# Kernel optimization log

Hardware: AMD Instinct MI355X
Metric: run time of the kernel (lower is better)

Reference implementation:

```python
import jax, jax.numpy as jnp
import numpy as np

C, PH, PW, H, W = 10, 7, 7, 34, 34
STRIDE = 8.0
S = 4  # sample_per_part


def setup_inputs() -> dict:
    key = jax.random.key(0)
    k1, k2, k3, k4, k5 = jax.random.split(key, 5)
    N = 30000
    ft = jax.random.normal(k1, (1, C * PH * PW, H, W), dtype=jnp.float32)
    x1 = jax.random.uniform(k2, (N,), dtype=jnp.float32) * 200.0
    y1 = jax.random.uniform(k3, (N,), dtype=jnp.float32) * 200.0
    bw = jax.random.uniform(k4, (N,), dtype=jnp.float32) * 70.0 + 2.0
    bh = jax.random.uniform(k5, (N,), dtype=jnp.float32) * 70.0 + 2.0
    rois = jnp.stack([jnp.zeros((N,), jnp.float32), x1, y1, x1 + bw, y1 + bh], axis=1)
    return {"ft_add_left_right": ft, "rois": rois}


def reference(ft_add_left_right, rois):
    ft = ft_add_left_right[0].reshape(C, PH, PW, H, W)
    roi_start_w = rois[:, 1] / STRIDE
    roi_start_h = rois[:, 2] / STRIDE
    roi_end_w = rois[:, 3] / STRIDE
    roi_end_h = rois[:, 4] / STRIDE
    # torch.threshold(x, 0.1, 0.1): x if x > 0.1 else 0.1
    roi_height = jnp.where(roi_end_h - roi_start_h > 0.1, roi_end_h - roi_start_h, 0.1)
    roi_width = jnp.where(roi_end_w - roi_start_w > 0.1, roi_end_w - roi_start_w, 0.1)
    bin_size_h = roi_height / PH
    bin_size_w = roi_width / PW
    sub_h = bin_size_h / S
    sub_w = bin_size_w / S

    gh, gw = jnp.meshgrid(jnp.arange(PH), jnp.arange(PW), indexing='ij')
    phs = gh.reshape(-1, 1)  # [49,1]
    pws = gw.reshape(-1, 1)  # [49,1]
    hstart = jnp.floor(roi_start_h + phs * bin_size_h)  # [49,N]
    wstart = jnp.floor(roi_start_w + pws * bin_size_w)  # [49,N]

    N = rois.shape[0]
    sum_ = jnp.zeros((C, PH * PW, N), jnp.float32)
    count = jnp.zeros((PH * PW, N), jnp.float32)

    for ih in range(S):
        for iw in range(S):
            w = wstart + (iw + 0.5) * sub_w  # [49,N]
            h = hstart + (ih + 0.5) * sub_h
            keep = (w > -1) & (w < W) & (h > -1) & (h < H)
            x1 = jnp.floor(w).astype(jnp.int32)
            x2 = jnp.ceil(w).astype(jnp.int32)
            y1 = jnp.floor(h).astype(jnp.int32)
            y2 = jnp.ceil(h).astype(jnp.int32)
            x1v = (x1 >= 0) & (x1 < W)
            x2v = (x2 >= 0) & (x2 < W)
            y1v = (y1 >= 0) & (y1 < H)
            y2v = (y2 >= 0) & (y2 < H)
            x1 = jnp.clip(x1, 0, W - 1)
            x2 = jnp.clip(x2, 0, W - 1)
            y1 = jnp.clip(y1, 0, H - 1)
            y2 = jnp.clip(y2, 0, H - 1)
            dist_x = w - x1
            dist_y = h - y1
            # gathers: result [C,49,N]
            v11 = ft[:, phs, pws, y1, x1]
            v12 = ft[:, phs, pws, y2, x1]
            v21 = ft[:, phs, pws, y1, x2]
            v22 = ft[:, phs, pws, y2, x2]
            # faithful to source: ALL four masks zero value11 only (source bug)
            bad11 = (~x1v & y1v) | (~x1v & y2v) | (~x2v & y1v) | (~x2v & y2v)
            v11 = jnp.where(bad11, 0.0, v11)
            value = ((1 - dist_x) * (1 - dist_y) * v11
                     + (1 - dist_x) * dist_y * v12
                     + dist_x * (1 - dist_y) * v21
                     + dist_x * dist_y * v22)
            sum_ = sum_ + jnp.where(keep, value, 0.0)
            count = count + keep.astype(jnp.float32)

    out = jnp.where(count > 0, sum_ / jnp.maximum(count, 1.0), sum_)
    return jnp.transpose(out, (2, 0, 1))  # [N, C, 49]
```

## Files before the change

### kernel.cpp

```cpp
#include <hip/hip_runtime.h>
#include <hip/hip_fp16.h>


#define NC 10
#define NBIN 49
#define FH 34
#define FW 34
#define PLANE (FH * FW)
#define NPIX (NBIN * PLANE)
#define GPC 18882
#define RPB 16
#define TSTRIDE 491
#define NSIDE 14

__global__ __launch_bounds__(256) void prep_kernel(
    const float* __restrict__ ft, unsigned int* __restrict__ ftR)
{
    const int p = blockIdx.x * 256 + threadIdx.x;
    if (p >= NPIX + 2) return;
    unsigned int h2[5];
    if (p < NPIX) {
#pragma unroll
        for (int c = 0; c < 5; ++c) {
            const __half lo = __float2half_rn(ft[(2 * c)     * NPIX + p]);
            const __half hi = __float2half_rn(ft[(2 * c + 1) * NPIX + p]);
            const __half2 hh = __halves2half2(lo, hi);
            h2[c] = *(const unsigned int*)&hh;
        }
    } else {
#pragma unroll
        for (int c = 0; c < 5; ++c) h2[c] = 0u;
    }
#pragma unroll
    for (int m = 0; m < 3; ++m) {
        if (p >= m) {
            const int t = p - m;
            const int g = t / 3;
            const int j = t - 3 * g;
            if (g < GPC) {
                unsigned int* d = ftR + ((size_t)m * GPC + g) * 16 + j * 5;
#pragma unroll
                for (int c = 0; c < 5; ++c) d[c] = h2[c];
            }
        }
    }
}

__device__ __forceinline__ void fma2(float w, unsigned int u, float& s0, float& s1)
{
    const __half2 h = *(const __half2*)&u;
    s0 = fmaf(w, __half2float(__low2half(h)),  s0);
    s1 = fmaf(w, __half2float(__high2half(h)), s1);
}

__global__ __launch_bounds__(256, 4) void main_kernel(
    const float* __restrict__ rois, const unsigned int* __restrict__ ftR,
    const float* __restrict__ ft, float* __restrict__ out, int N, int use_t)
{
    __shared__ float sides[NSIDE][RPB][8];
    __shared__ float tile[RPB][TSTRIDE];

    const int r = threadIdx.x & (RPB - 1);
    const int s = threadIdx.x >> 4;
    const int n = blockIdx.x * RPB + r;
    const bool valid = (n < N);

    float rsw = 0.f, rsh = 0.f, rew = 0.f, reh = 0.f;
    if (valid) {
        rsw = rois[n * 5 + 1] * 0.125f;
        rsh = rois[n * 5 + 2] * 0.125f;
        rew = rois[n * 5 + 3] * 0.125f;
        reh = rois[n * 5 + 4] * 0.125f;
    }
    float rheight = __fsub_rn(reh, rsh);
    if (!(rheight > 0.1f)) rheight = 0.1f;
    float rwidth = __fsub_rn(rew, rsw);
    if (!(rwidth > 0.1f)) rwidth = 0.1f;
    const float bsh   = __fdiv_rn(rheight, 7.0f);
    const float bsw   = __fdiv_rn(rwidth, 7.0f);
    const float sub_h = __fdiv_rn(bsh, 4.0f);
    const float sub_w = __fdiv_rn(bsw, 4.0f);

    if (s < NSIDE) {
        const bool isY = (s < 7);
        const int  k   = isY ? s : s - 7;
        const float st = isY ? rsh : rsw;
        const float bs = isY ? bsh : bsw;
        const float sb = isY ? sub_h : sub_w;
        const float start = floorf(__fadd_rn(st, __fmul_rn((float)k, bs)));

        float A[3] = {0.f, 0.f, 0.f}, B[3] = {0.f, 0.f, 0.f};
        float cnt = 0.f;
        int P0 = 0;
#pragma unroll
        for (int i = 0; i < 4; ++i) {
            const float h = __fadd_rn(start, __fmul_rn((float)i + 0.5f, sb));
            const bool ok = (h > -1.0f) && (h < 34.0f);
            const int p1 = (int)floorf(h);
            const int p2 = (int)ceilf(h);
            const bool v1 = (p1 >= 0) && (p1 < 34);
            const bool v2 = (p2 >= 0) && (p2 < 34);
            const int p1c = min(max(p1, 0), 33);
            const int p2c = min(max(p2, 0), 33);
            const float d = __fsub_rn(h, (float)p1c);
            if (i == 0) P0 = p1c;
            const int i1 = p1c - P0, i2 = p2c - P0;
            const float t1 = ok ? (1.0f - d) : 0.0f;
            const float t2 = ok ? d : 0.0f;
            const bool bsel = isY ? (v1 || v2) : ((!v1) || (!v2));
            const float tb = (ok && bsel) ? (1.0f - d) : 0.0f;
            cnt += ok ? 1.0f : 0.0f;
#pragma unroll
            for (int p = 0; p < 3; ++p) {
                A[p] += (i1 == p) ? t1 : 0.0f;
                A[p] += (i2 == p) ? t2 : 0.0f;
                B[p] += (i1 == p) ? tb : 0.0f;
            }
        }
        float* sp = &sides[s][r][0];
        sp[0] = A[0]; sp[1] = A[1]; sp[2] = A[2];
        sp[3] = B[0]; sp[4] = B[1]; sp[5] = B[2];
        sp[6] = cnt;  sp[7] = (float)P0;
    }
    __syncthreads();

#pragma unroll
    for (int j = 0; j < 4; ++j) {
        const int bin = j * RPB + s;
        if (valid && bin < NBIN) {
            const int ph = bin / 7;
            const int pw = bin - ph * 7;

            const float4 ya = *(const float4*)&sides[ph][r][0];
            const float4 yb = *(const float4*)&sides[ph][r][4];
            const float4 xa = *(const float4*)&sides[7 + pw][r][0];
            const float4 xb = *(const float4*)&sides[7 + pw][r][4];
            const float AY[3] = {ya.x, ya.y, ya.z};
            const float BY[3] = {ya.w, yb.x, yb.y};
            const float cntY  = yb.z;
            const int   Y0    = (int)yb.w;
            const float AX[3] = {xa.x, xa.y, xa.z};
            const float BX[3] = {xa.w, xb.x, xb.y};
            const float cntX  = xb.z;
            const int   X0    = (int)xb.w;

            const int binbase = bin * PLANE;
            const int rowo[3] = {binbase + Y0 * FW,
                                 binbase + min(Y0 + 1, FH - 1) * FW,
                                 binbase + min(Y0 + 2, FH - 1) * FW};

            float wgt[9];
#pragma unroll
            for (int p = 0; p < 3; ++p)
#pragma unroll
                for (int q = 0; q < 3; ++q)
                    wgt[3 * p + q] = AY[p] * AX[q] - BY[p] * BX[q];

            float sum[NC];
#pragma unroll
            for (int c = 0; c < NC; ++c) sum[c] = 0.f;

            if (use_t) {
                const int e = (FW - 1) - X0;
                unsigned int rv[3][15];
                float ew[3][3];
#pragma unroll
                for (int p = 0; p < 3; ++p) {
                    const float w0 = wgt[3 * p], w1 = wgt[3 * p + 1], w2 = wgt[3 * p + 2];
                    const float s12 = w1 + w2;
                    ew[p][0] = (e < 1) ? (w0 + s12) : w0;
                    ew[p][1] = (e < 1) ? 0.f : ((e < 2) ? s12 : w1);
                    ew[p][2] = (e < 2) ? 0.f : w2;
                    const bool rnz = (w0 != 0.0f) || (w1 != 0.0f) || (w2 != 0.0f);
                    const int fp = rnz ? (rowo[p] + X0) : binbase;
                    const int g = fp / 3;
                    const int m = fp - 3 * g;
                    const unsigned int* lp = ftR + ((size_t)m * GPC + g) * 16;
                    const uint4 a = *(const uint4*)lp;
                    const uint4 b = *(const uint4*)(lp + 4);
                    const uint4 c4 = *(const uint4*)(lp + 8);
                    const uint4 d4 = *(const uint4*)(lp + 12);
                    rv[p][0]  = a.x;  rv[p][1]  = a.y;  rv[p][2]  = a.z;  rv[p][3]  = a.w;
                    rv[p][4]  = b.x;  rv[p][5]  = b.y;  rv[p][6]  = b.z;  rv[p][7]  = b.w;
                    rv[p][8]  = c4.x; rv[p][9]  = c4.y; rv[p][10] = c4.z; rv[p][11] = c4.w;
                    rv[p][12] = d4.x; rv[p][13] = d4.y; rv[p][14] = d4.z;
                }
#pragma unroll
                for (int p = 0; p < 3; ++p)
#pragma unroll
                    for (int c = 0; c < 5; ++c) {
                        fma2(ew[p][0], rv[p][c],      sum[2 * c], sum[2 * c + 1]);
                        fma2(ew[p][1], rv[p][5 + c],  sum[2 * c], sum[2 * c + 1]);
                        fma2(ew[p][2], rv[p][10 + c], sum[2 * c], sum[2 * c + 1]);
                    }
            } else {
                const int colo[3] = {X0, min(X0 + 1, FW - 1), min(X0 + 2, FW - 1)};
                int off[9];
#pragma unroll
                for (int p = 0; p < 3; ++p)
#pragma unroll
                    for (int q = 0; q < 3; ++q)
                        off[3 * p + q] = (wgt[3 * p + q] != 0.0f) ? (rowo[p] + colo[q])
                                                                  : binbase;
#pragma unroll
                for (int k = 0; k < 9; ++k) {
                    const float w = wgt[k];
#pragma unroll
                    for (int c = 0; c < NC; ++c)
                        sum[c] = fmaf(w, ft[c * NPIX + off[k]], sum[c]);
                }
            }

            const float cnt = cntY * cntX;
            const float inv = (cnt > 0.0f) ? __fdiv_rn(1.0f, cnt) : 1.0f;
            float* tp = &tile[r][0];
#pragma unroll
            for (int c = 0; c < NC; ++c) tp[c * NBIN + bin] = sum[c] * inv;
        }
    }

    __syncthreads();

    const int n0 = blockIdx.x * RPB;
    for (int i = threadIdx.x; i < RPB * (NC * NBIN); i += 256) {
        const int row = i / (NC * NBIN);
        const int col = i - row * (NC * NBIN);
        const int n2 = n0 + row;
        if (n2 < N) out[(size_t)n2 * (NC * NBIN) + col] = tile[row][col];
    }
}

extern "C" void kernel_launch(void* const* d_in, const int* in_sizes, int n_in,
                              void* d_out, int out_size, void* d_ws, size_t ws_size,
                              hipStream_t stream) {
    const float* ft   = (const float*)d_in[0];
    const float* rois = (const float*)d_in[1];
    float* out        = (float*)d_out;
    const int N = in_sizes[1] / 5;

    const size_t need = (size_t)3 * GPC * 64;
    const int use_t = (ws_size >= need) ? 1 : 0;
    unsigned int* ftR = (unsigned int*)d_ws;

    if (use_t) {
        prep_kernel<<<(NPIX + 2 + 255) / 256, 256, 0, stream>>>(ft, ftR);
    }
    main_kernel<<<(N + RPB - 1) / RPB, 256, 0, stream>>>(rois, ftR, ft, out, N, use_t);
}
```

Measured before the change: 114.8 us.

## Sort ROIs by spatial key and remap blocks per XCD for cache locality

Adds a counting sort of ROIs keyed on start cell, half-cell parity and size class (histogram, scan, scatter kernels), so each block processes spatially similar ROIs. Block indices are also remapped so that consecutive sorted ranges land on the same XCD, which is meant to improve L2 reuse of the gathered feature data. The cost is four extra small kernel launches, a single-block serial scan, and output rows now written scattered through the permutation instead of contiguously.

```diff
diff --git a/kernel.cpp b/kernel.cpp
--- a/kernel.cpp
+++ b/kernel.cpp
@@ -12,6 +12,8 @@
 #define RPB 16
 #define TSTRIDE 491
 #define NSIDE 14
+#define NBUCKET 65536
+#define NXCD 8
 
 __global__ __launch_bounds__(256) void prep_kernel(
     const float* __restrict__ ft, unsigned int* __restrict__ ftR)
@@ -46,6 +48,71 @@
     }
 }
 
+__device__ __forceinline__ unsigned int roi_key(const float* __restrict__ rois, int n)
+{
+    const float rsw = rois[n * 5 + 1] * 0.125f;
+    const float rsh = rois[n * 5 + 2] * 0.125f;
+    const float rew = rois[n * 5 + 3] * 0.125f;
+    const float reh = rois[n * 5 + 4] * 0.125f;
+    float rh = reh - rsh; if (!(rh > 0.1f)) rh = 0.1f;
+    float rw = rew - rsw; if (!(rw > 0.1f)) rw = 0.1f;
+    const int y0 = min(31, max(0, (int)floorf(rsh)));
+    const int x0 = min(31, max(0, (int)floorf(rsw)));
+    const int yf = ((int)floorf(rsh * 2.0f)) & 1;
+    const int xf = ((int)floorf(rsw * 2.0f)) & 1;
+    const int bh = min(3, (int)(rh * (2.0f / 7.0f)));
+    const int bw = min(3, (int)(rw * (2.0f / 7.0f)));
+    return (unsigned int)((((((((y0 << 5) | x0) << 1) | yf) << 1) | xf) << 2 | bh) << 2 | bw);
+}
+
+__global__ __launch_bounds__(256) void zero_kernel(unsigned int* __restrict__ cursor)
+{
+    cursor[blockIdx.x * 256 + threadIdx.x] = 0u;
+}
+
+__global__ __launch_bounds__(256) void hist_kernel(
+    const float* __restrict__ rois, unsigned int* __restrict__ keys,
+    unsigned int* __restrict__ cursor, int N)
+{
+    const int n = blockIdx.x * 256 + threadIdx.x;
+    if (n >= N) return;
+    const unsigned int k = roi_key(rois, n);
+    keys[n] = k;
+    atomicAdd(&cursor[k], 1u);
+}
+
+__global__ __launch_bounds__(1024) void scan_kernel(unsigned int* __restrict__ cursor)
+{
+    __shared__ unsigned int part[1024];
+    const int t = threadIdx.x;
+    unsigned int s = 0;
+    for (int i = 0; i < 64; ++i) s += cursor[t * 64 + i];
+    part[t] = s;
+    __syncthreads();
+    for (int off = 1; off < 1024; off <<= 1) {
+        const unsigned int v = (t >= off) ? part[t - off] : 0u;
+        __syncthreads();
+        part[t] += v;
+        __syncthreads();
+    }
+    unsigned int ex = (t == 0) ? 0u : part[t - 1];
+    for (int i = 0; i < 64; ++i) {
+        const unsigned int c = cursor[t * 64 + i];
+        cursor[t * 64 + i] = ex;
+        ex += c;
+    }
+}
+
+__global__ __launch_bounds__(256) void scatter_kernel(
+    const unsigned int* __restrict__ keys, unsigned int* __restrict__ cursor,
+    int* __restrict__ perm, int N)
+{
+    const int n = blockIdx.x * 256 + threadIdx.x;
+    if (n >= N) return;
+    const unsigned int pos = atomicAdd(&cursor[keys[n]], 1u);
+    perm[pos] = n;
+}
+
 __device__ __forceinline__ void fma2(float w, unsigned int u, float& s0, float& s1)
 {
     const __half2 h = *(const __half2*)&u;
@@ -55,22 +122,29 @@
 
 __global__ __launch_bounds__(256, 4) void main_kernel(
     const float* __restrict__ rois, const unsigned int* __restrict__ ftR,
-    const float* __restrict__ ft, float* __restrict__ out, int N, int use_t)
+    const int* __restrict__ perm, const float* __restrict__ ft,
+    float* __restrict__ out, int N, int use_t)
 {
     __shared__ float sides[NSIDE][RPB][8];
     __shared__ float tile[RPB][TSTRIDE];
 
+    const int nwg = gridDim.x;
+    const int q = nwg / NXCD, rr = nwg % NXCD;
+    const int xcd = blockIdx.x % NXCD, idx = blockIdx.x / NXCD;
+    const int bid = (xcd < rr ? xcd * (q + 1) : rr * (q + 1) + (xcd - rr) * q) + idx;
+
     const int r = threadIdx.x & (RPB - 1);
     const int s = threadIdx.x >> 4;
-    const int n = blockIdx.x * RPB + r;
+    const int n = bid * RPB + r;
     const bool valid = (n < N);
+    const int nn = (use_t && valid) ? perm[n] : n;
 
     float rsw = 0.f, rsh = 0.f, rew = 0.f, reh = 0.f;
     if (valid) {
-        rsw = rois[n * 5 + 1] * 0.125f;
-        rsh = rois[n * 5 + 2] * 0.125f;
-        rew = rois[n * 5 + 3] * 0.125f;
-        reh = rois[n * 5 + 4] * 0.125f;
+        rsw = rois[nn * 5 + 1] * 0.125f;
+        rsh = rois[nn * 5 + 2] * 0.125f;
+        rew = rois[nn * 5 + 3] * 0.125f;
+        reh = rois[nn * 5 + 4] * 0.125f;
     }
     float rheight = __fsub_rn(reh, rsh);
     if (!(rheight > 0.1f)) rheight = 0.1f;
@@ -153,8 +227,8 @@
 #pragma unroll
             for (int p = 0; p < 3; ++p)
 #pragma unroll
-                for (int q = 0; q < 3; ++q)
-                    wgt[3 * p + q] = AY[p] * AX[q] - BY[p] * BX[q];
+                for (int q2 = 0; q2 < 3; ++q2)
+                    wgt[3 * p + q2] = AY[p] * AX[q2] - BY[p] * BX[q2];
 
             float sum[NC];
 #pragma unroll
@@ -199,9 +273,9 @@
 #pragma unroll
                 for (int p = 0; p < 3; ++p)
 #pragma unroll
-                    for (int q = 0; q < 3; ++q)
-                        off[3 * p + q] = (wgt[3 * p + q] != 0.0f) ? (rowo[p] + colo[q])
-                                                                  : binbase;
+                    for (int q2 = 0; q2 < 3; ++q2)
+                        off[3 * p + q2] = (wgt[3 * p + q2] != 0.0f) ? (rowo[p] + colo[q2])
+                                                                    : binbase;
 #pragma unroll
                 for (int k = 0; k < 9; ++k) {
                     const float w = wgt[k];
@@ -221,12 +295,15 @@
 
     __syncthreads();
 
-    const int n0 = blockIdx.x * RPB;
+    const int n0 = bid * RPB;
     for (int i = threadIdx.x; i < RPB * (NC * NBIN); i += 256) {
         const int row = i / (NC * NBIN);
         const int col = i - row * (NC * NBIN);
         const int n2 = n0 + row;
-        if (n2 < N) out[(size_t)n2 * (NC * NBIN) + col] = tile[row][col];
+        if (n2 < N) {
+            const int nd = use_t ? perm[n2] : n2;
+            out[(size_t)nd * (NC * NBIN) + col] = tile[row][col];
+        }
     }
 }
 
@@ -238,12 +315,20 @@
     float* out        = (float*)d_out;
     const int N = in_sizes[1] / 5;
 
-    const size_t need = (size_t)3 * GPC * 64;
+    const size_t ftr_bytes = (size_t)3 * GPC * 64;
+    const size_t need = ftr_bytes + (size_t)NBUCKET * 4 + (size_t)8 * N;
     const int use_t = (ws_size >= need) ? 1 : 0;
-    unsigned int* ftR = (unsigned int*)d_ws;
+    unsigned int* ftR    = (unsigned int*)d_ws;
+    unsigned int* cursor = (unsigned int*)((char*)d_ws + ftr_bytes);
+    unsigned int* keys   = cursor + NBUCKET;
+    int*          perm   = (int*)(keys + N);
 
     if (use_t) {
         prep_kernel<<<(NPIX + 2 + 255) / 256, 256, 0, stream>>>(ft, ftR);
-    }
-    main_kernel<<<(N + RPB - 1) / RPB, 256, 0, stream>>>(rois, ftR, ft, out, N, use_t);
-}
+        zero_kernel<<<NBUCKET / 256, 256, 0, stream>>>(cursor);
+        hist_kernel<<<(N + 255) / 256, 256, 0, stream>>>(rois, keys, cursor, N);
+        scan_kernel<<<1, 1024, 0, stream>>>(cursor);
+        scatter_kernel<<<(N + 255) / 256, 256, 0, stream>>>(keys, cursor, perm, N);
+    }
+    main_kernel<<<(N + RPB - 1) / RPB, 256, 0, stream>>>(rois, ftR, perm, ft, out, N, use_t);
+}
```

Result: slower. 144.9 us (+26.2%).

## Software-pipeline bin gathers with double-buffered registers and reduce occupancy hint

Applied to the files above, without the earlier changes.

Restructures the per-thread bin loop into a two-stage software pipeline. The gather loads for the next bin are issued before the FMAs of the current bin, using A/B register buffers, so global-memory latency overlaps with arithmetic. Invalid bins are handled by masking the weights and pointing at offset zero, which removes divergent branches around the loads. In exchange, register pressure goes up, so the launch-bounds minimum blocks per SM drops from 4 to 3. The prep kernel also moves to 1024-thread blocks.

```diff
diff --git a/kernel.cpp b/kernel.cpp
--- a/kernel.cpp
+++ b/kernel.cpp
@@ -13,11 +13,9 @@
 #define TSTRIDE 491
 #define NSIDE 14
 
-__global__ __launch_bounds__(256) void prep_kernel(
-    const float* __restrict__ ft, unsigned int* __restrict__ ftR)
-{
-    const int p = blockIdx.x * 256 + threadIdx.x;
-    if (p >= NPIX + 2) return;
+__device__ __forceinline__ void pack_pixel(
+    const float* __restrict__ ft, unsigned int* __restrict__ ftR, int p)
+{
     unsigned int h2[5];
     if (p < NPIX) {
 #pragma unroll
@@ -46,6 +44,13 @@
     }
 }
 
+__global__ __launch_bounds__(1024) void prep_kernel(
+    const float* __restrict__ ft, unsigned int* __restrict__ ftR)
+{
+    const int p = blockIdx.x * 1024 + threadIdx.x;
+    if (p < NPIX + 2) pack_pixel(ft, ftR, p);
+}
+
 __device__ __forceinline__ void fma2(float w, unsigned int u, float& s0, float& s1)
 {
     const __half2 h = *(const __half2*)&u;
@@ -53,7 +58,77 @@
     s1 = fmaf(w, __half2float(__high2half(h)), s1);
 }
 
-__global__ __launch_bounds__(256, 4) void main_kernel(
+
+#define BIN_META(J, EW, FP, INV, BINV, BVV)                                    \
+    {                                                                          \
+        BINV = (J) * RPB + s;                                                  \
+        BVV = valid && (BINV < NBIN);                                          \
+        const float msk = BVV ? 1.0f : 0.0f;                                   \
+        const int ph = BINV / 7;                                               \
+        const int pw = BINV - ph * 7;                                          \
+        const float4 ya = *(const float4*)&sides[ph][r][0];                    \
+        const float4 yb = *(const float4*)&sides[ph][r][4];                    \
+        const float4 xa = *(const float4*)&sides[7 + pw][r][0];                \
+        const float4 xb = *(const float4*)&sides[7 + pw][r][4];                \
+        const float AY[3] = {ya.x, ya.y, ya.z};                                \
+        const float BY[3] = {ya.w, yb.x, yb.y};                                \
+        const float AX[3] = {xa.x, xa.y, xa.z};                                \
+        const float BX[3] = {xa.w, xb.x, xb.y};                                \
+        const int Y0 = (int)yb.w;                                              \
+        const int X0 = (int)xb.w;                                              \
+        const float cnt = yb.z * xb.z;                                         \
+        INV = (cnt > 0.0f) ? __fdiv_rn(1.0f, cnt) : 1.0f;                      \
+        const int binbase = BINV * PLANE;                                      \
+        const int rowo[3] = {binbase + Y0 * FW,                                \
+                             binbase + min(Y0 + 1, FH - 1) * FW,               \
+                             binbase + min(Y0 + 2, FH - 1) * FW};              \
+        const int e = (FW - 1) - X0;                                           \
+        _Pragma("unroll") for (int p = 0; p < 3; ++p) {                        \
+            const float w0 = (AY[p] * AX[0] - BY[p] * BX[0]) * msk;            \
+            const float w1 = (AY[p] * AX[1] - BY[p] * BX[1]) * msk;            \
+            const float w2 = (AY[p] * AX[2] - BY[p] * BX[2]) * msk;            \
+            const float s12 = w1 + w2;                                         \
+            EW[p][0] = (e < 1) ? (w0 + s12) : w0;                              \
+            EW[p][1] = (e < 1) ? 0.f : ((e < 2) ? s12 : w1);                   \
+            EW[p][2] = (e < 2) ? 0.f : w2;                                     \
+            const bool rnz = (w0 != 0.0f) || (w1 != 0.0f) || (w2 != 0.0f);     \
+            FP[p] = BVV ? (rnz ? (rowo[p] + X0) : binbase) : 0;                \
+        }                                                                      \
+    }
+
+#define LOAD3(FP, RV)                                                          \
+    _Pragma("unroll") for (int p = 0; p < 3; ++p) {                            \
+        const int g = FP[p] / 3;                                               \
+        const int m = FP[p] - 3 * g;                                           \
+        const unsigned int* lp = ftR + ((size_t)m * GPC + g) * 16;             \
+        const uint4 a = *(const uint4*)lp;                                     \
+        const uint4 b4 = *(const uint4*)(lp + 4);                              \
+        const uint4 c4 = *(const uint4*)(lp + 8);                              \
+        const uint4 d4 = *(const uint4*)(lp + 12);                             \
+        RV[p][0] = a.x;  RV[p][1] = a.y;  RV[p][2] = a.z;  RV[p][3] = a.w;     \
+        RV[p][4] = b4.x; RV[p][5] = b4.y; RV[p][6] = b4.z; RV[p][7] = b4.w;    \
+        RV[p][8] = c4.x; RV[p][9] = c4.y; RV[p][10] = c4.z; RV[p][11] = c4.w;  \
+        RV[p][12] = d4.x; RV[p][13] = d4.y; RV[p][14] = d4.z;    \
+    }
+
+#define FMA_STORE(EW, RV, INV, BINV, BVV)                                      \
+    {                                                                          \
+        float sum[NC];                                                         \
+        _Pragma("unroll") for (int c = 0; c < NC; ++c) sum[c] = 0.f;           \
+        _Pragma("unroll") for (int p = 0; p < 3; ++p)                          \
+            _Pragma("unroll") for (int c = 0; c < 5; ++c) {                    \
+                fma2(EW[p][0], RV[p][c],      sum[2 * c], sum[2 * c + 1]);     \
+                fma2(EW[p][1], RV[p][5 + c],  sum[2 * c], sum[2 * c + 1]);     \
+                fma2(EW[p][2], RV[p][10 + c], sum[2 * c], sum[2 * c + 1]);     \
+            }                                                                  \
+        if (BVV) {                                                             \
+            float* tp = &tile[r][0];                                           \
+            _Pragma("unroll") for (int c = 0; c < NC; ++c)                     \
+                tp[c * NBIN + BINV] = sum[c] * INV;                            \
+        }                                                                      \
+    }
+
+__global__ __launch_bounds__(256, 3) void main_kernel(
     const float* __restrict__ rois, const unsigned int* __restrict__ ftR,
     const float* __restrict__ ft, float* __restrict__ out, int N, int use_t)
 {
@@ -124,84 +199,61 @@
     }
     __syncthreads();
 
-#pragma unroll
-    for (int j = 0; j < 4; ++j) {
-        const int bin = j * RPB + s;
-        if (valid && bin < NBIN) {
-            const int ph = bin / 7;
-            const int pw = bin - ph * 7;
-
-            const float4 ya = *(const float4*)&sides[ph][r][0];
-            const float4 yb = *(const float4*)&sides[ph][r][4];
-            const float4 xa = *(const float4*)&sides[7 + pw][r][0];
-            const float4 xb = *(const float4*)&sides[7 + pw][r][4];
-            const float AY[3] = {ya.x, ya.y, ya.z};
-            const float BY[3] = {ya.w, yb.x, yb.y};
-            const float cntY  = yb.z;
-            const int   Y0    = (int)yb.w;
-            const float AX[3] = {xa.x, xa.y, xa.z};
-            const float BX[3] = {xa.w, xb.x, xb.y};
-            const float cntX  = xb.z;
-            const int   X0    = (int)xb.w;
-
-            const int binbase = bin * PLANE;
-            const int rowo[3] = {binbase + Y0 * FW,
-                                 binbase + min(Y0 + 1, FH - 1) * FW,
-                                 binbase + min(Y0 + 2, FH - 1) * FW};
-
-            float wgt[9];
-#pragma unroll
-            for (int p = 0; p < 3; ++p)
-#pragma unroll
-                for (int q = 0; q < 3; ++q)
-                    wgt[3 * p + q] = AY[p] * AX[q] - BY[p] * BX[q];
-
-            float sum[NC];
-#pragma unroll
-            for (int c = 0; c < NC; ++c) sum[c] = 0.f;
-
-            if (use_t) {
-                const int e = (FW - 1) - X0;
-                unsigned int rv[3][15];
-                float ew[3][3];
-#pragma unroll
-                for (int p = 0; p < 3; ++p) {
-                    const float w0 = wgt[3 * p], w1 = wgt[3 * p + 1], w2 = wgt[3 * p + 2];
-                    const float s12 = w1 + w2;
-                    ew[p][0] = (e < 1) ? (w0 + s12) : w0;
-                    ew[p][1] = (e < 1) ? 0.f : ((e < 2) ? s12 : w1);
-                    ew[p][2] = (e < 2) ? 0.f : w2;
-                    const bool rnz = (w0 != 0.0f) || (w1 != 0.0f) || (w2 != 0.0f);
-                    const int fp = rnz ? (rowo[p] + X0) : binbase;
-                    const int g = fp / 3;
-                    const int m = fp - 3 * g;
-                    const unsigned int* lp = ftR + ((size_t)m * GPC + g) * 16;
-                    const uint4 a = *(const uint4*)lp;
-                    const uint4 b = *(const uint4*)(lp + 4);
-                    const uint4 c4 = *(const uint4*)(lp + 8);
-                    const uint4 d4 = *(const uint4*)(lp + 12);
-                    rv[p][0]  = a.x;  rv[p][1]  = a.y;  rv[p][2]  = a.z;  rv[p][3]  = a.w;
-                    rv[p][4]  = b.x;  rv[p][5]  = b.y;  rv[p][6]  = b.z;  rv[p][7]  = b.w;
-                    rv[p][8]  = c4.x; rv[p][9]  = c4.y; rv[p][10] = c4.z; rv[p][11] = c4.w;
-                    rv[p][12] = d4.x; rv[p][13] = d4.y; rv[p][14] = d4.z;
-                }
+    if (use_t) {
+        float ewA[3][3], ewB[3][3];
+        int   fpA[3], fpB[3];
+        float invA, invB;
+        int   binA, binB;
+        bool  bvA, bvB;
+        unsigned int rvA[3][15], rvB[3][15];
+
+        BIN_META(0, ewA, fpA, invA, binA, bvA);
+        LOAD3(fpA, rvA);
+        BIN_META(1, ewB, fpB, invB, binB, bvB);
+        LOAD3(fpB, rvB);
+        FMA_STORE(ewA, rvA, invA, binA, bvA);
+        BIN_META(2, ewA, fpA, invA, binA, bvA);
+        LOAD3(fpA, rvA);
+        FMA_STORE(ewB, rvB, invB, binB, bvB);
+        BIN_META(3, ewB, fpB, invB, binB, bvB);
+        LOAD3(fpB, rvB);
+        FMA_STORE(ewA, rvA, invA, binA, bvA);
+        FMA_STORE(ewB, rvB, invB, binB, bvB);
+    } else {
+#pragma unroll
+        for (int j = 0; j < 4; ++j) {
+            const int bin = j * RPB + s;
+            if (valid && bin < NBIN) {
+                const int ph = bin / 7;
+                const int pw = bin - ph * 7;
+                const float4 ya = *(const float4*)&sides[ph][r][0];
+                const float4 yb = *(const float4*)&sides[ph][r][4];
+                const float4 xa = *(const float4*)&sides[7 + pw][r][0];
+                const float4 xb = *(const float4*)&sides[7 + pw][r][4];
+                const float AY[3] = {ya.x, ya.y, ya.z};
+                const float BY[3] = {ya.w, yb.x, yb.y};
+                const float AX[3] = {xa.x, xa.y, xa.z};
+                const float BX[3] = {xa.w, xb.x, xb.y};
+                const int Y0 = (int)yb.w, X0 = (int)xb.w;
+                const float cnt = yb.z * xb.z;
+                const int binbase = bin * PLANE;
+                const int rowo[3] = {binbase + Y0 * FW,
+                                     binbase + min(Y0 + 1, FH - 1) * FW,
+                                     binbase + min(Y0 + 2, FH - 1) * FW};
+                const int colo[3] = {X0, min(X0 + 1, FW - 1), min(X0 + 2, FW - 1)};
+                float wgt[9];
+                int off[9];
 #pragma unroll
                 for (int p = 0; p < 3; ++p)
 #pragma unroll
-                    for (int c = 0; c < 5; ++c) {
-                        fma2(ew[p][0], rv[p][c],      sum[2 * c], sum[2 * c + 1]);
-                        fma2(ew[p][1], rv[p][5 + c],  sum[2 * c], sum[2 * c + 1]);
-                        fma2(ew[p][2], rv[p][10 + c], sum[2 * c], sum[2 * c + 1]);
+                    for (int q2 = 0; q2 < 3; ++q2) {
+                        const float w = AY[p] * AX[q2] - BY[p] * BX[q2];
+                        wgt[3 * p + q2] = w;
+                        off[3 * p + q2] = (w != 0.0f) ? (rowo[p] + colo[q2]) : binbase;
                     }
-            } else {
-                const int colo[3] = {X0, min(X0 + 1, FW - 1), min(X0 + 2, FW - 1)};
-                int off[9];
-#pragma unroll
-                for (int p = 0; p < 3; ++p)
-#pragma unroll
-                    for (int q = 0; q < 3; ++q)
-                        off[3 * p + q] = (wgt[3 * p + q] != 0.0f) ? (rowo[p] + colo[q])
-                                                                  : binbase;
+                float sum[NC];
+#pragma unroll
+                for (int c = 0; c < NC; ++c) sum[c] = 0.f;
 #pragma unroll
                 for (int k = 0; k < 9; ++k) {
                     const float w = wgt[k];
@@ -209,13 +261,11 @@
                     for (int c = 0; c < NC; ++c)
                         sum[c] = fmaf(w, ft[c * NPIX + off[k]], sum[c]);
                 }
+                const float inv = (cnt > 0.0f) ? __fdiv_rn(1.0f, cnt) : 1.0f;
+                float* tp = &tile[r][0];
+#pragma unroll
+                for (int c = 0; c < NC; ++c) tp[c * NBIN + bin] = sum[c] * inv;
             }
-
-            const float cnt = cntY * cntX;
-            const float inv = (cnt > 0.0f) ? __fdiv_rn(1.0f, cnt) : 1.0f;
-            float* tp = &tile[r][0];
-#pragma unroll
-            for (int c = 0; c < NC; ++c) tp[c * NBIN + bin] = sum[c] * inv;
         }
     }
 
@@ -243,7 +293,7 @@
     unsigned int* ftR = (unsigned int*)d_ws;
 
     if (use_t) {
-        prep_kernel<<<(NPIX + 2 + 255) / 256, 256, 0, stream>>>(ft, ftR);
+        prep_kernel<<<(NPIX + 2 + 1023) / 1024, 1024, 0, stream>>>(ft, ftR);
     }
     main_kernel<<<(N + RPB - 1) / RPB, 256, 0, stream>>>(rois, ftR, ft, out, N, use_t);
 }
```

New measurement: 114.3 us. Within noise of the previous version (-0.4%).

## Split bin gather across 16 lanes per ROI with shuffle reduction

Applied to the files above, without the earlier changes.

Restructures the packed-fp16 gather path so that each ROI is handled by a 16-lane group that loops over all 49 bins. Each lane loads a single 32-bit word (one column offset and channel pair) per row, instead of each thread loading three 64-byte rows per bin. Partial sums across the three column offsets are combined with wave shuffles, and only five lanes write to the shared tile. The prep kernel now uses 1024-thread blocks and zeroes the padding word, and the occupancy hint on the main kernel is dropped. The aim is to cut per-thread register pressure and uncoalesced wide loads, at the cost of more shuffles and serialized bin loops.

```diff
diff --git a/kernel.cpp b/kernel.cpp
--- a/kernel.cpp
+++ b/kernel.cpp
@@ -13,11 +13,9 @@
 #define TSTRIDE 491
 #define NSIDE 14
 
-__global__ __launch_bounds__(256) void prep_kernel(
-    const float* __restrict__ ft, unsigned int* __restrict__ ftR)
-{
-    const int p = blockIdx.x * 256 + threadIdx.x;
-    if (p >= NPIX + 2) return;
+__device__ __forceinline__ void pack_pixel(
+    const float* __restrict__ ft, unsigned int* __restrict__ ftR, int p)
+{
     unsigned int h2[5];
     if (p < NPIX) {
 #pragma unroll
@@ -41,9 +39,17 @@
                 unsigned int* d = ftR + ((size_t)m * GPC + g) * 16 + j * 5;
 #pragma unroll
                 for (int c = 0; c < 5; ++c) d[c] = h2[c];
-            }
-        }
-    }
+                if (j == 0) d[15] = 0u;
+            }
+        }
+    }
+}
+
+__global__ __launch_bounds__(1024) void prep_kernel(
+    const float* __restrict__ ft, unsigned int* __restrict__ ftR)
+{
+    const int p = blockIdx.x * 1024 + threadIdx.x;
+    if (p < NPIX + 2) pack_pixel(ft, ftR, p);
 }
 
 __device__ __forceinline__ void fma2(float w, unsigned int u, float& s0, float& s1)
@@ -53,7 +59,7 @@
     s1 = fmaf(w, __half2float(__high2half(h)), s1);
 }
 
-__global__ __launch_bounds__(256, 4) void main_kernel(
+__global__ __launch_bounds__(256) void main_kernel(
     const float* __restrict__ rois, const unsigned int* __restrict__ ftR,
     const float* __restrict__ ft, float* __restrict__ out, int N, int use_t)
 {
@@ -124,84 +130,105 @@
     }
     __syncthreads();
 
-#pragma unroll
-    for (int j = 0; j < 4; ++j) {
-        const int bin = j * RPB + s;
-        if (valid && bin < NBIN) {
-            const int ph = bin / 7;
-            const int pw = bin - ph * 7;
-
-            const float4 ya = *(const float4*)&sides[ph][r][0];
-            const float4 yb = *(const float4*)&sides[ph][r][4];
-            const float4 xa = *(const float4*)&sides[7 + pw][r][0];
-            const float4 xb = *(const float4*)&sides[7 + pw][r][4];
-            const float AY[3] = {ya.x, ya.y, ya.z};
-            const float BY[3] = {ya.w, yb.x, yb.y};
-            const float cntY  = yb.z;
-            const int   Y0    = (int)yb.w;
-            const float AX[3] = {xa.x, xa.y, xa.z};
-            const float BX[3] = {xa.w, xb.x, xb.y};
-            const float cntX  = xb.z;
-            const int   X0    = (int)xb.w;
-
-            const int binbase = bin * PLANE;
-            const int rowo[3] = {binbase + Y0 * FW,
-                                 binbase + min(Y0 + 1, FH - 1) * FW,
-                                 binbase + min(Y0 + 2, FH - 1) * FW};
-
-            float wgt[9];
-#pragma unroll
-            for (int p = 0; p < 3; ++p)
-#pragma unroll
-                for (int q = 0; q < 3; ++q)
-                    wgt[3 * p + q] = AY[p] * AX[q] - BY[p] * BX[q];
-
-            float sum[NC];
-#pragma unroll
-            for (int c = 0; c < NC; ++c) sum[c] = 0.f;
-
-            if (use_t) {
-                const int e = (FW - 1) - X0;
-                unsigned int rv[3][15];
-                float ew[3][3];
-#pragma unroll
-                for (int p = 0; p < 3; ++p) {
-                    const float w0 = wgt[3 * p], w1 = wgt[3 * p + 1], w2 = wgt[3 * p + 2];
-                    const float s12 = w1 + w2;
-                    ew[p][0] = (e < 1) ? (w0 + s12) : w0;
-                    ew[p][1] = (e < 1) ? 0.f : ((e < 2) ? s12 : w1);
-                    ew[p][2] = (e < 2) ? 0.f : w2;
-                    const bool rnz = (w0 != 0.0f) || (w1 != 0.0f) || (w2 != 0.0f);
-                    const int fp = rnz ? (rowo[p] + X0) : binbase;
-                    const int g = fp / 3;
-                    const int m = fp - 3 * g;
-                    const unsigned int* lp = ftR + ((size_t)m * GPC + g) * 16;
-                    const uint4 a = *(const uint4*)lp;
-                    const uint4 b = *(const uint4*)(lp + 4);
-                    const uint4 c4 = *(const uint4*)(lp + 8);
-                    const uint4 d4 = *(const uint4*)(lp + 12);
-                    rv[p][0]  = a.x;  rv[p][1]  = a.y;  rv[p][2]  = a.z;  rv[p][3]  = a.w;
-                    rv[p][4]  = b.x;  rv[p][5]  = b.y;  rv[p][6]  = b.z;  rv[p][7]  = b.w;
-                    rv[p][8]  = c4.x; rv[p][9]  = c4.y; rv[p][10] = c4.z; rv[p][11] = c4.w;
-                    rv[p][12] = d4.x; rv[p][13] = d4.y; rv[p][14] = d4.z;
-                }
+    if (use_t) {
+        const int L   = threadIdx.x & 63;
+        const int wv  = threadIdx.x >> 6;
+        const int grp = L >> 4;
+        const int rr  = wv * 4 + grp;
+        const int t   = L & 15;
+        const int q   = t / 5;
+        const int cp  = t - q * 5;
+        const int n2  = blockIdx.x * RPB + rr;
+        const bool vroi = (n2 < N);
+        const float msk = (vroi && t != 15) ? 1.0f : 0.0f;
+
+        for (int ph = 0; ph < 7; ++ph) {
+            const float4 ya = *(const float4*)&sides[ph][rr][0];
+            const float4 yb = *(const float4*)&sides[ph][rr][4];
+            const int   Y0  = (int)yb.w;
+            const int   yo0 = Y0 * FW;
+            const int   yo1 = min(Y0 + 1, FH - 1) * FW;
+            const int   yo2 = min(Y0 + 2, FH - 1) * FW;
+            const float cy  = yb.z;
+
+            for (int pw = 0; pw < 7; ++pw) {
+                const int bin = ph * 7 + pw;
+                const float4 xa = *(const float4*)&sides[7 + pw][rr][0];
+                const float4 xb = *(const float4*)&sides[7 + pw][rr][4];
+                const int X0 = (int)xb.w;
+                const int e  = (FW - 1) - X0;
+                const float cnt = cy * xb.z;
+                const float inv = (cnt > 0.0f) ? __fdiv_rn(1.0f, cnt) : 1.0f;
+                const float axq = (q == 0) ? xa.x : ((q == 1) ? xa.y : xa.z);
+                const float bxq = (q == 0) ? xa.w : ((q == 1) ? xb.x : xb.y);
+                const int   d   = min(q, e) * 5 + cp;
+                const int  base = bin * PLANE + X0;
+
+                float s0 = 0.f, s1 = 0.f;
+                {
+                    const float w = (ya.x * axq - ya.w * bxq) * msk;
+                    const int fp = vroi ? (base + yo0) : 0;
+                    const int g = fp / 3;  const int m = fp - 3 * g;
+                    fma2(w, ftR[((size_t)(m * GPC + g) << 4) + d], s0, s1);
+                }
+                {
+                    const float w = (ya.y * axq - yb.x * bxq) * msk;
+                    const int fp = vroi ? (base + yo1) : 0;
+                    const int g = fp / 3;  const int m = fp - 3 * g;
+                    fma2(w, ftR[((size_t)(m * GPC + g) << 4) + d], s0, s1);
+                }
+                {
+                    const float w = (ya.z * axq - yb.y * bxq) * msk;
+                    const int fp = vroi ? (base + yo2) : 0;
+                    const int g = fp / 3;  const int m = fp - 3 * g;
+                    fma2(w, ftR[((size_t)(m * GPC + g) << 4) + d], s0, s1);
+                }
+                const float r0 = s0 + __shfl(s0, (L + 5) & 63, 64)
+                                    + __shfl(s0, (L + 10) & 63, 64);
+                const float r1 = s1 + __shfl(s1, (L + 5) & 63, 64)
+                                    + __shfl(s1, (L + 10) & 63, 64);
+                if (vroi && t < 5) {
+                    float* tp = &tile[rr][0];
+                    tp[(2 * cp) * NBIN + bin]     = r0 * inv;
+                    tp[(2 * cp + 1) * NBIN + bin] = r1 * inv;
+                }
+            }
+        }
+    } else {
+#pragma unroll
+        for (int j = 0; j < 4; ++j) {
+            const int bin = j * RPB + s;
+            if (valid && bin < NBIN) {
+                const int ph = bin / 7;
+                const int pw = bin - ph * 7;
+                const float4 ya = *(const float4*)&sides[ph][r][0];
+                const float4 yb = *(const float4*)&sides[ph][r][4];
+                const float4 xa = *(const float4*)&sides[7 + pw][r][0];
+                const float4 xb = *(const float4*)&sides[7 + pw][r][4];
+                const float AY[3] = {ya.x, ya.y, ya.z};
+                const float BY[3] = {ya.w, yb.x, yb.y};
+                const float AX[3] = {xa.x, xa.y, xa.z};
+                const float BX[3] = {xa.w, xb.x, xb.y};
+                const int Y0 = (int)yb.w, X0 = (int)xb.w;
+                const float cnt = yb.z * xb.z;
+                const int binbase = bin * PLANE;
+                const int rowo[3] = {binbase + Y0 * FW,
+                                     binbase + min(Y0 + 1, FH - 1) * FW,
+                                     binbase + min(Y0 + 2, FH - 1) * FW};
+                const int colo[3] = {X0, min(X0 + 1, FW - 1), min(X0 + 2, FW - 1)};
+                float wgt[9];
+                int off[9];
 #pragma unroll
                 for (int p = 0; p < 3; ++p)
 #pragma unroll
-                    for (int c = 0; c < 5; ++c) {
-                        fma2(ew[p][0], rv[p][c],      sum[2 * c], sum[2 * c + 1]);
-                        fma2(ew[p][1], rv[p][5 + c],  sum[2 * c], sum[2 * c + 1]);
-                        fma2(ew[p][2], rv[p][10 + c], sum[2 * c], sum[2 * c + 1]);
+                    for (int q2 = 0; q2 < 3; ++q2) {
+                        const float w = AY[p] * AX[q2] - BY[p] * BX[q2];
+                        wgt[3 * p + q2] = w;
+                        off[3 * p + q2] = (w != 0.0f) ? (rowo[p] + colo[q2]) : binbase;
                     }
-            } else {
-                const int colo[3] = {X0, min(X0 + 1, FW - 1), min(X0 + 2, FW - 1)};
-                int off[9];
-#pragma unroll
-                for (int p = 0; p < 3; ++p)
-#pragma unroll
-                    for (int q = 0; q < 3; ++q)
-                        off[3 * p + q] = (wgt[3 * p + q] != 0.0f) ? (rowo[p] + colo[q])
-                                                                  : binbase;
+                float sum[NC];
+#pragma unroll
+                for (int c = 0; c < NC; ++c) sum[c] = 0.f;
 #pragma unroll
                 for (int k = 0; k < 9; ++k) {
                     const float w = wgt[k];
@@ -209,13 +236,11 @@
                     for (int c = 0; c < NC; ++c)
                         sum[c] = fmaf(w, ft[c * NPIX + off[k]], sum[c]);
                 }
-            }
-
-            const float cnt = cntY * cntX;
-            const float inv = (cnt > 0.0f) ? __fdiv_rn(1.0f, cnt) : 1.0f;
-            float* tp = &tile[r][0];
-#pragma unroll
-            for (int c = 0; c < NC; ++c) tp[c * NBIN + bin] = sum[c] * inv;
+                const float inv = (cnt > 0.0f) ? __fdiv_rn(1.0f, cnt) : 1.0f;
+                float* tp = &tile[r][0];
+#pragma unroll
+                for (int c = 0; c < NC; ++c) tp[c * NBIN + bin] = sum[c] * inv;
+            }
         }
     }
 
@@ -243,7 +268,7 @@
     unsigned int* ftR = (unsigned int*)d_ws;
 
     if (use_t) {
-        prep_kernel<<<(NPIX + 2 + 255) / 256, 256, 0, stream>>>(ft, ftR);
+        prep_kernel<<<(NPIX + 2 + 1023) / 1024, 1024, 0, stream>>>(ft, ftR);
     }
     main_kernel<<<(N + RPB - 1) / RPB, 256, 0, stream>>>(rois, ftR, ft, out, N, use_t);
 }
```

New measurement: 136.7 us. 1.19x slower.
